# Performance work log

Hardware: AMD Instinct MI355X
Metric: run time of the kernel (lower is better)

The kernel has to match this reference:

```python
import jax, jax.numpy as jnp
import numpy as np

N, IN_F, OUT_F = 8192, 512, 256
NEG_INF = -9e15
LEAKY_SLOPE = 0.25


def setup_inputs() -> dict:
    key = jax.random.key(0)
    k1, k2, k3, k4, k5, k6 = jax.random.split(key, 6)
    inp = {
        "input": jax.random.normal(k1, (N, IN_F), dtype=jnp.float32),
        "adj": jax.random.randint(k2, (N, N), 0, 2, dtype=jnp.int32),
        # learned params (xavier-normal-ish scale)
        "weights": jax.random.normal(k3, (IN_F, OUT_F), dtype=jnp.float32) * (2.0 / (IN_F + OUT_F)) ** 0.5,
        "a1": jax.random.normal(k4, (OUT_F, 1), dtype=jnp.float32) * (2.0 / (OUT_F + 1)) ** 0.5,
        "a2": jax.random.normal(k5, (OUT_F, 1), dtype=jnp.float32) * (2.0 / (OUT_F + 1)) ** 0.5,
        "bias": jax.random.uniform(k6, (OUT_F,), dtype=jnp.float32, minval=-1.0 / OUT_F ** 0.5, maxval=1.0 / OUT_F ** 0.5),
    }
    return inp


def reference(input, adj, weights, a1, a2, bias):
    # h = input @ W  : [N, out]
    h = input @ weights
    # e[i,j] = leaky_relu((h@a1)[i] + (h@a2)[j])  : [N, N] via broadcast
    e1 = h @ a1  # [N,1]
    e2 = h @ a2  # [N,1]
    e = e1 + e2.T
    e = jnp.where(e > 0, e, LEAKY_SLOPE * e)
    # mask non-edges, row softmax (dropout omitted: deterministic reference)
    scores = jnp.where(adj > 0, e, NEG_INF)
    attention = jax.nn.softmax(scores, axis=1)
    # aggregate + bias
    return attention @ h + bias
```

## Files before the change

kernel.cpp:

```cpp
#include <hip/hip_runtime.h>

typedef __attribute__((ext_vector_type(8))) short short8;
typedef __attribute__((ext_vector_type(4))) float floatx4;
typedef __attribute__((ext_vector_type(4))) unsigned int uintx4;
typedef __attribute__((ext_vector_type(2))) unsigned int uintx2;
typedef __attribute__((ext_vector_type(4))) int intx4;
typedef __attribute__((ext_vector_type(4))) unsigned short ushortx4;
typedef unsigned int u32;

#define NN 8192
#define KIN 512
#define COUT 256
#define SHIFT 16.0f

#define AS1 __attribute__((address_space(1)))
#define AS3 __attribute__((address_space(3)))

__device__ __forceinline__ void stage16(const void* g, void* l) {
  __builtin_amdgcn_global_load_lds((const AS1 u32*)g, (AS3 u32*)l, 16, 0, 0);
}

__device__ __forceinline__ unsigned int f2bf(float f) {
  unsigned int u = __float_as_uint(f);
  return (u + 0x7FFFu + ((u >> 16) & 1u)) >> 16;
}

__device__ __forceinline__ short8 pack8(const float* p) {
  uintx4 w;
  w.x = f2bf(p[0]) | (f2bf(p[1]) << 16);
  w.y = f2bf(p[2]) | (f2bf(p[3]) << 16);
  w.z = f2bf(p[4]) | (f2bf(p[5]) << 16);
  w.w = f2bf(p[6]) | (f2bf(p[7]) << 16);
  union { uintx4 u; short8 s; } cv; cv.u = w;
  return cv.s;
}

__global__ __launch_bounds__(256)
void k_compress(const int* __restrict__ adj, unsigned int* __restrict__ bm) {
  int idx = blockIdx.x * 256 + threadIdx.x;
  const int* p = adj + (size_t)idx * 32;
  unsigned int m = 0;
#pragma unroll
  for (int k = 0; k < 8; ++k) {
    intx4 v = *(const intx4*)(p + k * 4);
    m |= (v.x != 0 ? 1u : 0u) << (k * 4 + 0);
    m |= (v.y != 0 ? 1u : 0u) << (k * 4 + 1);
    m |= (v.z != 0 ? 1u : 0u) << (k * 4 + 2);
    m |= (v.w != 0 ? 1u : 0u) << (k * 4 + 3);
  }
  bm[idx] = m;
}

__global__ void k_cast_input(const float* __restrict__ in, ushortx4* __restrict__ out) {
  int idx = blockIdx.x * 256 + threadIdx.x;
  floatx4 v = ((const floatx4*)in)[idx];
  ushortx4 o;
  o.x = (unsigned short)f2bf(v.x);
  o.y = (unsigned short)f2bf(v.y);
  o.z = (unsigned short)f2bf(v.z);
  o.w = (unsigned short)f2bf(v.w);
  out[idx] = o;
}

__global__ void k_prep_w(const float* __restrict__ w, unsigned short* __restrict__ wt) {
  int idx = blockIdx.x * 256 + threadIdx.x;
  int k = idx >> 8, c = idx & 255;
  wt[c * KIN + k] = (unsigned short)f2bf(w[idx]);
}

__global__ __launch_bounds__(256)
void k_gemm_h(const unsigned short* __restrict__ inA, const unsigned short* __restrict__ wt,
              const float* __restrict__ a1, const float* __restrict__ a2,
              unsigned short* __restrict__ ht, float* __restrict__ e1, float* __restrict__ e2) {
  int wave = threadIdx.x >> 6;
  int lane = threadIdx.x & 63;
  int n = lane & 15, q = lane >> 4;
  int row0 = blockIdx.x * 64 + wave * 16;
  int mrow = row0 + n;

  floatx4 acc[16];
#pragma unroll
  for (int t = 0; t < 16; ++t) acc[t] = (floatx4){0.f, 0.f, 0.f, 0.f};

  for (int kc = 0; kc < KIN / 32; ++kc) {
    int k0 = kc * 32 + q * 8;
    short8 a = *(const short8*)(inA + (size_t)mrow * KIN + k0);
#pragma unroll
    for (int nt = 0; nt < 16; ++nt) {
      short8 b = *(const short8*)(wt + (size_t)(nt * 16 + n) * KIN + k0);
      acc[nt] = __builtin_amdgcn_mfma_f32_16x16x32_bf16(a, b, acc[nt], 0, 0, 0);
    }
  }

  int i0 = row0 + q * 4;
#pragma unroll
  for (int nt = 0; nt < 16; ++nt) {
    int c = nt * 16 + n;
    uintx2 pk;
    pk.x = f2bf(acc[nt][0]) | (f2bf(acc[nt][1]) << 16);
    pk.y = f2bf(acc[nt][2]) | (f2bf(acc[nt][3]) << 16);
    *(uintx2*)(ht + (size_t)c * NN + i0) = pk;
  }

  float s1[4] = {0.f, 0.f, 0.f, 0.f}, s2[4] = {0.f, 0.f, 0.f, 0.f};
#pragma unroll
  for (int nt = 0; nt < 16; ++nt) {
    float w1 = a1[nt * 16 + n];
    float w2 = a2[nt * 16 + n];
#pragma unroll
    for (int r = 0; r < 4; ++r) {
      s1[r] += acc[nt][r] * w1;
      s2[r] += acc[nt][r] * w2;
    }
  }
#pragma unroll
  for (int m = 1; m < 16; m <<= 1) {
#pragma unroll
    for (int r = 0; r < 4; ++r) {
      s1[r] += __shfl_xor(s1[r], m);
      s2[r] += __shfl_xor(s2[r], m);
    }
  }
  if (n == 0) {
#pragma unroll
    for (int r = 0; r < 4; ++r) {
      e1[i0 + r] = s1[r];
      e2[i0 + r] = s2[r];
    }
  }
}

__global__ __launch_bounds__(256, 2)
void k_attn_part(const unsigned int* __restrict__ bm, const unsigned short* __restrict__ ht,
                 const float* __restrict__ e1, const float* __restrict__ e2,
                 float* __restrict__ opart, float* __restrict__ Dpart) {
  __shared__ __align__(16) char smem[32768];

  int b = blockIdx.x;
  int rg = b >> 3, js = b & 7;
  int wave = threadIdx.x >> 6, lane = threadIdx.x & 63;
  int n = lane & 15, q = lane >> 4;
  int rowbase = rg * 128 + wave * 32;
  int jbeg = js * 1024;

  float e1v0 = e1[rowbase + n];
  float e1v1 = e1[rowbase + 16 + n];

  const unsigned int* bp0 = bm + (size_t)(rowbase + n) * 256 + js * 32;
  const unsigned int* bp1 = bm + (size_t)(rowbase + 16 + n) * 256 + js * 32;

  floatx4 acc[2][16];
#pragma unroll
  for (int t = 0; t < 2; ++t)
#pragma unroll
    for (int nt = 0; nt < 16; ++nt) acc[t][nt] = (floatx4){0.f, 0.f, 0.f, 0.f};

  float d0 = 0.f, d1 = 0.f;

  auto stage = [&](int ch, int buf) {
    int j0g = jbeg + ch * 32;
    int segbase = wave * 256;
#pragma unroll
    for (int i = 0; i < 4; ++i) {
      int seg = segbase + i * 64 + lane;
      int c = seg >> 2;
      int js8 = (seg & 3) * 8;
      stage16(ht + (size_t)c * NN + j0g + js8,
              smem + (size_t)buf * 16384 + (size_t)(segbase + i * 64) * 16);
    }
  };

  stage(0, 0);
  __syncthreads();

  for (int ch = 0; ch < 32; ++ch) {
    int cur = ch & 1;
    if (ch < 31) stage(ch + 1, cur ^ 1);

    int j0 = jbeg + ch * 32 + q * 8;
    floatx4 ea = *(const floatx4*)(e2 + j0);
    floatx4 eb = *(const floatx4*)(e2 + j0 + 4);
    float ev[8] = {ea.x, ea.y, ea.z, ea.w, eb.x, eb.y, eb.z, eb.w};

    unsigned int by0 = (bp0[ch] >> (q * 8)) & 0xffu;
    unsigned int by1 = (bp1[ch] >> (q * 8)) & 0xffu;

    float p0[8], p1[8];
#pragma unroll
    for (int jj = 0; jj < 8; ++jj) {
      float t0 = e1v0 + ev[jj];
      float t1 = e1v1 + ev[jj];
      float f0 = fmaxf(t0, 0.25f * t0);
      float f1 = fmaxf(t1, 0.25f * t1);
      float x0 = __expf(f0 - SHIFT);
      float x1 = __expf(f1 - SHIFT);
      p0[jj] = ((by0 >> jj) & 1u) ? x0 : 0.f;
      p1[jj] = ((by1 >> jj) & 1u) ? x1 : 0.f;
      d0 += p0[jj];
      d1 += p1[jj];
    }
    short8 af0 = pack8(p0);
    short8 af1 = pack8(p1);

    const short8* lb = (const short8*)(smem + (size_t)cur * 16384);
#pragma unroll
    for (int t = 0; t < 16; ++t) {
      short8 bf = lb[t * 64 + n * 4 + q];
      acc[0][t] = __builtin_amdgcn_mfma_f32_16x16x32_bf16(af0, bf, acc[0][t], 0, 0, 0);
      acc[1][t] = __builtin_amdgcn_mfma_f32_16x16x32_bf16(af1, bf, acc[1][t], 0, 0, 0);
    }

    __syncthreads();
  }

  d0 += __shfl_xor(d0, 16); d0 += __shfl_xor(d0, 32);
  d1 += __shfl_xor(d1, 16); d1 += __shfl_xor(d1, 32);
  if (lane < 16) {
    Dpart[(size_t)js * NN + rowbase + lane] = d0;
    Dpart[(size_t)js * NN + rowbase + 16 + lane] = d1;
  }

  float* op = opart + (size_t)js * NN * COUT;
#pragma unroll
  for (int t2 = 0; t2 < 2; ++t2) {
#pragma unroll
    for (int nt = 0; nt < 16; ++nt) {
#pragma unroll
      for (int r = 0; r < 4; ++r) {
        int i = rowbase + t2 * 16 + q * 4 + r;
        op[(size_t)i * COUT + nt * 16 + n] = acc[t2][nt][r];
      }
    }
  }
}

__global__ void k_final_part(float* __restrict__ out, const float* __restrict__ opart,
                             const float* __restrict__ Dpart, const float* __restrict__ bias) {
  int i = blockIdx.x;
  int c = threadIdx.x;
  float s = 0.f, d = 0.f;
#pragma unroll
  for (int js = 0; js < 8; ++js) {
    s += opart[((size_t)js * NN + i) * COUT + c];
    d += Dpart[(size_t)js * NN + i];
  }
  out[(size_t)i * COUT + c] = s / fmaxf(d, 1e-37f) + bias[c];
}

__global__ __launch_bounds__(256, 2)
void k_attn_atomic(const int* __restrict__ adj, const unsigned short* __restrict__ ht,
                   const float* __restrict__ e1, const float* __restrict__ e2,
                   float* __restrict__ out_num, float* __restrict__ Dbuf) {
  int b = blockIdx.x;
  int rg = b >> 3, js = b & 7;
  int wave = threadIdx.x >> 6, lane = threadIdx.x & 63;
  int n = lane & 15, q = lane >> 4;
  int rowbase = rg * 128 + wave * 32;

  float e1v0 = e1[rowbase + n];
  float e1v1 = e1[rowbase + 16 + n];

  floatx4 acc[2][16];
#pragma unroll
  for (int t = 0; t < 2; ++t)
#pragma unroll
    for (int nt = 0; nt < 16; ++nt) acc[t][nt] = (floatx4){0.f, 0.f, 0.f, 0.f};

  float d0 = 0.f, d1 = 0.f;
  int jbeg = js * 1024;

  for (int ch = 0; ch < 32; ++ch) {
    int j0 = jbeg + ch * 32 + q * 8;
    floatx4 ea = *(const floatx4*)(e2 + j0);
    floatx4 eb = *(const floatx4*)(e2 + j0 + 4);
    float ev[8] = {ea.x, ea.y, ea.z, ea.w, eb.x, eb.y, eb.z, eb.w};

    intx4 A00 = *(const intx4*)(adj + (size_t)(rowbase + n) * NN + j0);
    intx4 A01 = *(const intx4*)(adj + (size_t)(rowbase + n) * NN + j0 + 4);
    intx4 A10 = *(const intx4*)(adj + (size_t)(rowbase + 16 + n) * NN + j0);
    intx4 A11 = *(const intx4*)(adj + (size_t)(rowbase + 16 + n) * NN + j0 + 4);

    float p0[8], p1[8];
#pragma unroll
    for (int jj = 0; jj < 8; ++jj) {
      int av0 = (jj < 4) ? A00[jj] : A01[jj - 4];
      int av1 = (jj < 4) ? A10[jj] : A11[jj - 4];
      float t0 = e1v0 + ev[jj];
      float t1 = e1v1 + ev[jj];
      float f0 = fmaxf(t0, 0.25f * t0);
      float f1 = fmaxf(t1, 0.25f * t1);
      float x0 = __expf(f0 - SHIFT);
      float x1 = __expf(f1 - SHIFT);
      p0[jj] = (av0 != 0) ? x0 : 0.f;
      p1[jj] = (av1 != 0) ? x1 : 0.f;
      d0 += p0[jj];
      d1 += p1[jj];
    }
    short8 af0 = pack8(p0);
    short8 af1 = pack8(p1);

#pragma unroll
    for (int g = 0; g < 2; ++g) {
      short8 bf[8];
#pragma unroll
      for (int t = 0; t < 8; ++t)
        bf[t] = *(const short8*)(ht + (size_t)((g * 8 + t) * 16 + n) * NN + j0);
#pragma unroll
      for (int t = 0; t < 8; ++t) {
        acc[0][g * 8 + t] = __builtin_amdgcn_mfma_f32_16x16x32_bf16(af0, bf[t], acc[0][g * 8 + t], 0, 0, 0);
        acc[1][g * 8 + t] = __builtin_amdgcn_mfma_f32_16x16x32_bf16(af1, bf[t], acc[1][g * 8 + t], 0, 0, 0);
      }
    }
  }

  d0 += __shfl_xor(d0, 16); d0 += __shfl_xor(d0, 32);
  d1 += __shfl_xor(d1, 16); d1 += __shfl_xor(d1, 32);
  if (lane < 16) {
    atomicAdd(Dbuf + rowbase + lane, d0);
    atomicAdd(Dbuf + rowbase + 16 + lane, d1);
  }

#pragma unroll
  for (int t2 = 0; t2 < 2; ++t2) {
#pragma unroll
    for (int nt = 0; nt < 16; ++nt) {
#pragma unroll
      for (int r = 0; r < 4; ++r) {
        int i = rowbase + t2 * 16 + q * 4 + r;
        atomicAdd(out_num + (size_t)i * COUT + nt * 16 + n, acc[t2][nt][r]);
      }
    }
  }
}

__global__ void k_final_atomic(float* __restrict__ out, const float* __restrict__ Dbuf,
                               const float* __restrict__ bias) {
  int idx = blockIdx.x * 256 + threadIdx.x;
  int i = idx >> 8, c = idx & 255;
  float d = fmaxf(Dbuf[i], 1e-37f);
  out[idx] = out[idx] / d + bias[c];
}

extern "C" void kernel_launch(void* const* d_in, const int* in_sizes, int n_in,
                              void* d_out, int out_size, void* d_ws, size_t ws_size,
                              hipStream_t stream) {
  const float* input   = (const float*)d_in[0];
  const int*   adj     = (const int*)d_in[1];
  const float* weights = (const float*)d_in[2];
  const float* a1      = (const float*)d_in[3];
  const float* a2      = (const float*)d_in[4];
  const float* bias    = (const float*)d_in[5];
  float* out = (float*)d_out;
  char* ws = (char*)d_ws;

  unsigned short* inA = (unsigned short*)(ws);
  unsigned short* wt  = (unsigned short*)(ws + 8388608);
  unsigned short* ht  = (unsigned short*)(ws + 8650752);
  float* e1    = (float*)(ws + 12845056);
  float* e2    = (float*)(ws + 12877824);
  float* Dpart = (float*)(ws + 12910592);
  unsigned int* bm = (unsigned int*)(ws + 13172736);
  float* opart = (float*)(ws + 21561344);
  const size_t WS_NEEDED_PART = 21561344 + (size_t)8 * NN * COUT * 4;
  float* Dbuf = Dpart;

  if (ws_size >= WS_NEEDED_PART) {
    k_compress<<<8192, 256, 0, stream>>>(adj, bm);
    k_cast_input<<<4096, 256, 0, stream>>>(input, (ushortx4*)inA);
    k_prep_w<<<512, 256, 0, stream>>>(weights, wt);
    k_gemm_h<<<128, 256, 0, stream>>>(inA, wt, a1, a2, ht, e1, e2);
    k_attn_part<<<512, 256, 0, stream>>>(bm, ht, e1, e2, opart, Dpart);
    k_final_part<<<8192, 256, 0, stream>>>(out, opart, Dpart, bias);
  } else {
    k_cast_input<<<4096, 256, 0, stream>>>(input, (ushortx4*)inA);
    k_prep_w<<<512, 256, 0, stream>>>(weights, wt);
    k_gemm_h<<<128, 256, 0, stream>>>(inA, wt, a1, a2, ht, e1, e2);
    hipMemsetAsync(out, 0, (size_t)NN * COUT * sizeof(float), stream);
    hipMemsetAsync(Dbuf, 0, NN * sizeof(float), stream);
    k_attn_atomic<<<512, 256, 0, stream>>>(adj, ht, e1, e2, out, Dbuf);
    k_final_atomic<<<8192, 256, 0, stream>>>(out, Dbuf, bias);
  }
}
```

Baseline: 487.6 us.

## Fuse adjacency mask reading into attention kernel via async LDS staging

Removes the separate bitmask compression kernel. The attention kernel now streams raw int32 adjacency tiles into shared memory with global_load_lds, double-buffered alongside the h tiles, and caches the e2 slice in LDS. This cuts one full pass over the 256MB adjacency matrix plus the bitmask write and read. The cost is about 69KB of LDS per block, which may reduce occupancy below the requested 2 blocks/CU, and a wider per-chunk global load inside the main loop.

Measured after the change: 463.7 us. 1.05x faster.

```diff
diff --git a/kernel.cpp b/kernel.cpp
--- a/kernel.cpp
+++ b/kernel.cpp
@@ -33,22 +33,6 @@
   w.w = f2bf(p[6]) | (f2bf(p[7]) << 16);
   union { uintx4 u; short8 s; } cv; cv.u = w;
   return cv.s;
-}
-
-__global__ __launch_bounds__(256)
-void k_compress(const int* __restrict__ adj, unsigned int* __restrict__ bm) {
-  int idx = blockIdx.x * 256 + threadIdx.x;
-  const int* p = adj + (size_t)idx * 32;
-  unsigned int m = 0;
-#pragma unroll
-  for (int k = 0; k < 8; ++k) {
-    intx4 v = *(const intx4*)(p + k * 4);
-    m |= (v.x != 0 ? 1u : 0u) << (k * 4 + 0);
-    m |= (v.y != 0 ? 1u : 0u) << (k * 4 + 1);
-    m |= (v.z != 0 ? 1u : 0u) << (k * 4 + 2);
-    m |= (v.w != 0 ? 1u : 0u) << (k * 4 + 3);
-  }
-  bm[idx] = m;
 }
 
 __global__ void k_cast_input(const float* __restrict__ in, ushortx4* __restrict__ out) {
@@ -131,24 +115,25 @@
 }
 
 __global__ __launch_bounds__(256, 2)
-void k_attn_part(const unsigned int* __restrict__ bm, const unsigned short* __restrict__ ht,
-                 const float* __restrict__ e1, const float* __restrict__ e2,
-                 float* __restrict__ opart, float* __restrict__ Dpart) {
-  __shared__ __align__(16) char smem[32768];
+void k_attn_fused(const int* __restrict__ adj, const unsigned short* __restrict__ ht,
+                  const float* __restrict__ e1, const float* __restrict__ e2,
+                  float* __restrict__ opart, float* __restrict__ Dpart) {
+  __shared__ __align__(16) char smem[69632];
+  float* e2s = (float*)(smem + 65536);
 
   int b = blockIdx.x;
   int rg = b >> 3, js = b & 7;
   int wave = threadIdx.x >> 6, lane = threadIdx.x & 63;
   int n = lane & 15, q = lane >> 4;
-  int rowbase = rg * 128 + wave * 32;
+  int rowblock = rg * 128;
+  int rowbase = rowblock + wave * 32;
   int jbeg = js * 1024;
+
+  ((floatx4*)e2s)[threadIdx.x] = *(const floatx4*)(e2 + jbeg + threadIdx.x * 4);
 
   float e1v0 = e1[rowbase + n];
   float e1v1 = e1[rowbase + 16 + n];
 
-  const unsigned int* bp0 = bm + (size_t)(rowbase + n) * 256 + js * 32;
-  const unsigned int* bp1 = bm + (size_t)(rowbase + 16 + n) * 256 + js * 32;
-
   floatx4 acc[2][16];
 #pragma unroll
   for (int t = 0; t < 2; ++t)
@@ -159,50 +144,61 @@
 
   auto stage = [&](int ch, int buf) {
     int j0g = jbeg + ch * 32;
-    int segbase = wave * 256;
+    char* hbase = smem + buf * 32768;
 #pragma unroll
     for (int i = 0; i < 4; ++i) {
-      int seg = segbase + i * 64 + lane;
+      int seg = wave * 256 + i * 64 + lane;
       int c = seg >> 2;
-      int js8 = (seg & 3) * 8;
-      stage16(ht + (size_t)c * NN + j0g + js8,
-              smem + (size_t)buf * 16384 + (size_t)(segbase + i * 64) * 16);
+      int j8 = (seg & 3) * 8;
+      stage16(ht + (size_t)c * NN + j0g + j8, hbase + (size_t)(wave * 256 + i * 64) * 16);
+    }
+    char* abase = hbase + 16384 + wave * 4096;
+    const int* aw = adj + (size_t)(rowblock + wave * 32) * NN + j0g;
+#pragma unroll
+    for (int i = 0; i < 4; ++i) {
+      stage16(aw + (size_t)(i * 8 + (lane & 7)) * NN + (lane >> 3) * 4, abase + i * 1024);
     }
   };
 
   stage(0, 0);
   __syncthreads();
+
+  int rlo = n & 7, rhi = n >> 3;
 
   for (int ch = 0; ch < 32; ++ch) {
     int cur = ch & 1;
     if (ch < 31) stage(ch + 1, cur ^ 1);
 
-    int j0 = jbeg + ch * 32 + q * 8;
-    floatx4 ea = *(const floatx4*)(e2 + j0);
-    floatx4 eb = *(const floatx4*)(e2 + j0 + 4);
+    const char* ab = smem + cur * 32768 + 16384 + wave * 4096;
+    intx4 a0a = *(const intx4*)(ab + rhi * 1024 + q * 256 + rlo * 16);
+    intx4 a0b = *(const intx4*)(ab + rhi * 1024 + q * 256 + 128 + rlo * 16);
+    intx4 a1a = *(const intx4*)(ab + 2048 + rhi * 1024 + q * 256 + rlo * 16);
+    intx4 a1b = *(const intx4*)(ab + 2048 + rhi * 1024 + q * 256 + 128 + rlo * 16);
+
+    floatx4 ea = *(const floatx4*)(e2s + ch * 32 + q * 8);
+    floatx4 eb = *(const floatx4*)(e2s + ch * 32 + q * 8 + 4);
     float ev[8] = {ea.x, ea.y, ea.z, ea.w, eb.x, eb.y, eb.z, eb.w};
 
-    unsigned int by0 = (bp0[ch] >> (q * 8)) & 0xffu;
-    unsigned int by1 = (bp1[ch] >> (q * 8)) & 0xffu;
-
     float p0[8], p1[8];
 #pragma unroll
     for (int jj = 0; jj < 8; ++jj) {
+      int av0 = (jj < 4) ? a0a[jj] : a0b[jj - 4];
+      int av1 = (jj < 4) ? a1a[jj] : a1b[jj - 4];
       float t0 = e1v0 + ev[jj];
       float t1 = e1v1 + ev[jj];
       float f0 = fmaxf(t0, 0.25f * t0);
       float f1 = fmaxf(t1, 0.25f * t1);
       float x0 = __expf(f0 - SHIFT);
       float x1 = __expf(f1 - SHIFT);
-      p0[jj] = ((by0 >> jj) & 1u) ? x0 : 0.f;
-      p1[jj] = ((by1 >> jj) & 1u) ? x1 : 0.f;
+      p0[jj] = (av0 != 0) ? x0 : 0.f;
+      p1[jj] = (av1 != 0) ? x1 : 0.f;
       d0 += p0[jj];
       d1 += p1[jj];
     }
     short8 af0 = pack8(p0);
     short8 af1 = pack8(p1);
 
-    const short8* lb = (const short8*)(smem + (size_t)cur * 16384);
+    const short8* lb = (const short8*)(smem + (size_t)cur * 32768);
 #pragma unroll
     for (int t = 0; t < 16; ++t) {
       short8 bf = lb[t * 64 + n * 4 + q];
@@ -359,22 +355,18 @@
   float* e1    = (float*)(ws + 12845056);
   float* e2    = (float*)(ws + 12877824);
   float* Dpart = (float*)(ws + 12910592);
-  unsigned int* bm = (unsigned int*)(ws + 13172736);
-  float* opart = (float*)(ws + 21561344);
-  const size_t WS_NEEDED_PART = 21561344 + (size_t)8 * NN * COUT * 4;
+  float* opart = (float*)(ws + 13172736);
+  const size_t WS_NEEDED_PART = 13172736 + (size_t)8 * NN * COUT * 4;
   float* Dbuf = Dpart;
 
+  k_cast_input<<<4096, 256, 0, stream>>>(input, (ushortx4*)inA);
+  k_prep_w<<<512, 256, 0, stream>>>(weights, wt);
+  k_gemm_h<<<128, 256, 0, stream>>>(inA, wt, a1, a2, ht, e1, e2);
+
   if (ws_size >= WS_NEEDED_PART) {
-    k_compress<<<8192, 256, 0, stream>>>(adj, bm);
-    k_cast_input<<<4096, 256, 0, stream>>>(input, (ushortx4*)inA);
-    k_prep_w<<<512, 256, 0, stream>>>(weights, wt);
-    k_gemm_h<<<128, 256, 0, stream>>>(inA, wt, a1, a2, ht, e1, e2);
-    k_attn_part<<<512, 256, 0, stream>>>(bm, ht, e1, e2, opart, Dpart);
+    k_attn_fused<<<512, 256, 0, stream>>>(adj, ht, e1, e2, opart, Dpart);
     k_final_part<<<8192, 256, 0, stream>>>(out, opart, Dpart, bias);
   } else {
-    k_cast_input<<<4096, 256, 0, stream>>>(input, (ushortx4*)inA);
-    k_prep_w<<<512, 256, 0, stream>>>(weights, wt);
-    k_gemm_h<<<128, 256, 0, stream>>>(inA, wt, a1, a2, ht, e1, e2);
     hipMemsetAsync(out, 0, (size_t)NN * COUT * sizeof(float), stream);
     hipMemsetAsync(Dbuf, 0, NN * sizeof(float), stream);
     k_attn_atomic<<<512, 256, 0, stream>>>(adj, ht, e1, e2, out, Dbuf);
```
